# Performance work log

Hardware: AMD Instinct MI355X
Metric: run time of the kernel (lower is better)

## Reference

```python
import jax, jax.numpy as jnp
import numpy as np

D_MODEL = 256
NHEAD = 8
NUM_LAYERS = 4
LN_EPS = 1e-5

def _layernorm(x, g, b):
    mu = jnp.mean(x, axis=-1, keepdims=True)
    var = jnp.mean((x - mu) ** 2, axis=-1, keepdims=True)
    return (x - mu) * jax.lax.rsqrt(var + LN_EPS) * g + b

def setup_inputs() -> dict:
    key = jax.random.key(0)
    ks = jax.random.split(key, 16)
    B, M, D, L = 2, 2048, D_MODEL, NUM_LAYERS
    s = 0.02
    inp = {
        'x': jax.random.normal(ks[0], (B, M, D), jnp.float32),
        'coords': jax.random.normal(ks[1], (B, M, 3), jnp.float32),
        'wq': jax.random.normal(ks[2], (L, D, D), jnp.float32) * s,
        'bq': jnp.zeros((L, D), jnp.float32),
        'wk': jax.random.normal(ks[3], (L, D, D), jnp.float32) * s,
        'bk': jnp.zeros((L, D), jnp.float32),
        'wv': jax.random.normal(ks[4], (L, D, D), jnp.float32) * s,
        'bv': jnp.zeros((L, D), jnp.float32),
        'alpha': jnp.full((L,), 0.1, jnp.float32),
        'w1': jax.random.normal(ks[5], (L, D, 2 * D), jnp.float32) * s,
        'b1': jnp.zeros((L, 2 * D), jnp.float32),
        'w2': jax.random.normal(ks[6], (L, 2 * D, D), jnp.float32) * s,
        'b2': jnp.zeros((L, D), jnp.float32),
        'ln1_g': jnp.ones((L, D), jnp.float32),
        'ln1_b': jnp.zeros((L, D), jnp.float32),
        'ln2_g': jnp.ones((L, D), jnp.float32),
        'ln2_b': jnp.zeros((L, D), jnp.float32),
    }
    return inp

def reference(x, coords, wq, bq, wk, bk, wv, bv, alpha, w1, b1, w2, b2, ln1_g, ln1_b, ln2_g, ln2_b):
    B, M, D = x.shape
    H = NHEAD
    dk = D // H
    # Geometric bias: per-batch block of the original B*M x B*M dot matrix,
    # i.e. G[b] = coords[b] @ coords[b].T  (identical math, computed directly).
    G0 = jnp.einsum('bmd,bnd->bmn', coords, coords)  # [B, M, M]
    scale = 1.0 / jnp.sqrt(jnp.asarray(dk, x.dtype))

    def heads(t):  # [B,M,D] -> [B,H,M,dk]
        return t.reshape(B, M, H, dk).transpose(0, 2, 1, 3)

    for i in range(NUM_LAYERS):
        q = heads(x @ wq[i] + bq[i])
        k = heads(x @ wk[i] + bk[i])
        v = heads(x @ wv[i] + bv[i])
        scores = jnp.einsum('bhmd,bhnd->bhmn', q, k) * scale + (alpha[i] * G0)[:, None]
        attn = jax.nn.softmax(scores, axis=-1)
        out = jnp.einsum('bhmn,bhnd->bhmd', attn, v)
        out = out.transpose(0, 2, 1, 3).reshape(B, M, D)
        x = _layernorm(x + out, ln1_g[i], ln1_b[i])
        ff = jax.nn.relu(x @ w1[i] + b1[i]) @ w2[i] + b2[i]
        x = _layernorm(x + ff, ln2_g[i], ln2_b[i])
    return x
```

## Files before the change

kernel.cpp:

```cpp
#include <hip/hip_runtime.h>

typedef unsigned short u16;
typedef __attribute__((ext_vector_type(8))) short short8;
typedef __attribute__((ext_vector_type(4))) float f32x4;
typedef __attribute__((ext_vector_type(4))) u16 u16x4;

#define MFMA16(a, b, c) __builtin_amdgcn_mfma_f32_16x16x32_bf16(a, b, c, 0, 0, 0)
#define EXP2(x) __builtin_amdgcn_exp2f(x)

#define LOG2E 1.4426950408889634f
#define QSCALE 0.25506038410312156f

__device__ __forceinline__ u16 f2bf(float f) {
    unsigned int u = __builtin_bit_cast(unsigned int, f);
    u += 0x7fffu + ((u >> 16) & 1u);
    return (u16)(u >> 16);
}

__global__ __launch_bounds__(256) void repack_kernel(
    const float* __restrict__ wq, const float* __restrict__ wk, const float* __restrict__ wv,
    const float* __restrict__ bq, const float* __restrict__ bk, const float* __restrict__ bv,
    const float* __restrict__ w1, const float* __restrict__ w2,
    u16* __restrict__ wqkvT, u16* __restrict__ w1T, u16* __restrict__ w2T,
    float* __restrict__ bqkv)
{
    long idx = (long)blockIdx.x * 256 + threadIdx.x;
    const long NQ = 4L * 768 * 256;
    const long N1 = 4L * 512 * 256;
    const long N2 = 4L * 256 * 512;
    const long NB = 4L * 768;
    if (idx < NQ) {
        long l = idx / (768 * 256); long r = idx % (768 * 256);
        long n = r / 256, k = r % 256;
        float v;
        if (n < 256)      v = wq[(l * 256 + k) * 256 + n] * QSCALE;
        else if (n < 512) v = wk[(l * 256 + k) * 256 + (n - 256)];
        else              v = wv[(l * 256 + k) * 256 + (n - 512)];
        wqkvT[idx] = f2bf(v);
    } else if ((idx -= NQ) < N1) {
        long l = idx / (512 * 256); long r = idx % (512 * 256);
        long n = r / 256, k = r % 256;
        w1T[idx] = f2bf(w1[(l * 256 + k) * 512 + n]);
    } else if ((idx -= N1) < N2) {
        long l = idx / (256 * 512); long r = idx % (256 * 512);
        long n = r / 512, k = r % 512;
        w2T[idx] = f2bf(w2[(l * 512 + k) * 256 + n]);
    } else if ((idx -= N2) < NB) {
        long l = idx / 768; long n = idx % 768;
        float v = (n < 256) ? bq[l * 256 + n] * QSCALE
                : (n < 512) ? bk[l * 256 + (n - 256)]
                            : bv[l * 256 + (n - 512)];
        bqkv[l * 768 + n] = v;
    }
}

__global__ __launch_bounds__(256) void xconv_kernel(
    const float* __restrict__ xin, const float* __restrict__ coords,
    float* __restrict__ xf, u16* __restrict__ xb, u16* __restrict__ kcoord)
{
    long idx = (long)blockIdx.x * 256 + threadIdx.x;
    if (idx < 4096L * 256) {
        float v = xin[idx];
        xf[idx] = v;
        xb[idx] = f2bf(v);
    }
    if (idx < 4096) {
        const float* c = coords + idx * 3;
        u16 r0 = f2bf(c[0] * LOG2E), r1 = f2bf(c[1] * LOG2E), r2 = f2bf(c[2] * LOG2E);
        uint4 lo; lo.x = (unsigned)r0 | ((unsigned)r1 << 16); lo.y = (unsigned)r2; lo.z = 0; lo.w = 0;
        uint4 z4; z4.x = 0; z4.y = 0; z4.z = 0; z4.w = 0;
        uint4* dst = (uint4*)(kcoord + idx * 32);
        dst[0] = lo; dst[1] = z4; dst[2] = z4; dst[3] = z4;
    }
}

__global__ __launch_bounds__(256) void qkvgemm_kernel(
    const u16* __restrict__ A, const u16* __restrict__ BT,
    const float* __restrict__ bias,
    u16* __restrict__ qt, u16* __restrict__ kt, u16* __restrict__ vt)
{
    const int K = 256;
    int w = threadIdx.x >> 6, lane = threadIdx.x & 63;
    int wr = w >> 1, wc = w & 1;
    int m0 = blockIdx.x * 64 + wr * 32;
    int n0 = blockIdx.y * 64 + wc * 32;
    int l16 = lane & 15, lhi = lane >> 4;

    f32x4 acc[2][2];
#pragma unroll
    for (int i = 0; i < 2; i++)
#pragma unroll
        for (int j = 0; j < 2; j++) acc[i][j] = (f32x4){0.f, 0.f, 0.f, 0.f};

    const u16* Ap = A + (size_t)(m0 + l16) * K + lhi * 8;
    const u16* Bp = BT + (size_t)(n0 + l16) * K + lhi * 8;

#pragma unroll 4
    for (int k = 0; k < K; k += 32) {
        short8 a0 = *(const short8*)(Ap + k);
        short8 a1 = *(const short8*)(Ap + (size_t)16 * K + k);
        short8 b0 = *(const short8*)(Bp + k);
        short8 b1 = *(const short8*)(Bp + (size_t)16 * K + k);
        acc[0][0] = MFMA16(a0, b0, acc[0][0]);
        acc[0][1] = MFMA16(a0, b1, acc[0][1]);
        acc[1][0] = MFMA16(a1, b0, acc[1][0]);
        acc[1][1] = MFMA16(a1, b1, acc[1][1]);
    }

#pragma unroll
    for (int i = 0; i < 2; i++)
#pragma unroll
        for (int j = 0; j < 2; j++) {
            int n = n0 + j * 16 + l16;
            float bs = bias[n];
            int sect = n >> 8;
            int h = (n >> 5) & 7;
            int d = n & 31;
            int m = m0 + i * 16 + lhi * 4;
            int b = m >> 11, mseq = m & 2047;
            if (sect < 2) {
                u16* dst = (sect == 0 ? qt : kt) + ((size_t)(b * 8 + h) * 2048 + mseq) * 32 + d;
#pragma unroll
                for (int r = 0; r < 4; r++) dst[(size_t)r * 32] = f2bf(acc[i][j][r] + bs);
            } else {
                u16x4 pk;
#pragma unroll
                for (int r = 0; r < 4; r++) pk[r] = f2bf(acc[i][j][r] + bs);
                *(u16x4*)(vt + ((size_t)(b * 8 + h) * 32 + d) * 2048 + mseq) = pk;
            }
        }
}

template <bool RELU, bool OUTF32>
__global__ __launch_bounds__(256) void gemm_kernel(
    const u16* __restrict__ A, const u16* __restrict__ BT,
    const float* __restrict__ bias, void* __restrict__ outp,
    int M, int N, int K)
{
    int w = threadIdx.x >> 6, lane = threadIdx.x & 63;
    int wr = w >> 1, wc = w & 1;
    int m0 = blockIdx.x * 64 + wr * 32;
    int n0 = blockIdx.y * 64 + wc * 32;
    int l16 = lane & 15, lhi = lane >> 4;

    f32x4 acc[2][2];
#pragma unroll
    for (int i = 0; i < 2; i++)
#pragma unroll
        for (int j = 0; j < 2; j++) acc[i][j] = (f32x4){0.f, 0.f, 0.f, 0.f};

    const u16* Ap = A + (size_t)(m0 + l16) * K + lhi * 8;
    const u16* Bp = BT + (size_t)(n0 + l16) * K + lhi * 8;

#pragma unroll 4
    for (int k = 0; k < K; k += 32) {
        short8 a0 = *(const short8*)(Ap + k);
        short8 a1 = *(const short8*)(Ap + (size_t)16 * K + k);
        short8 b0 = *(const short8*)(Bp + k);
        short8 b1 = *(const short8*)(Bp + (size_t)16 * K + k);
        acc[0][0] = MFMA16(a0, b0, acc[0][0]);
        acc[0][1] = MFMA16(a0, b1, acc[0][1]);
        acc[1][0] = MFMA16(a1, b0, acc[1][0]);
        acc[1][1] = MFMA16(a1, b1, acc[1][1]);
    }

#pragma unroll
    for (int i = 0; i < 2; i++)
#pragma unroll
        for (int j = 0; j < 2; j++) {
            int n = n0 + j * 16 + l16;
            float bs = bias[n];
#pragma unroll
            for (int r = 0; r < 4; r++) {
                int m = m0 + i * 16 + lhi * 4 + r;
                float v = acc[i][j][r] + bs;
                if (RELU) v = fmaxf(v, 0.f);
                if (OUTF32) ((float*)outp)[(size_t)m * N + n] = v;
                else        ((u16*)outp)[(size_t)m * N + n] = f2bf(v);
            }
        }
}

__global__ __launch_bounds__(256, 4) void attn_kernel(
    const u16* __restrict__ qt, const u16* __restrict__ kt, const u16* __restrict__ vt,
    const u16* __restrict__ kcoord, const float* __restrict__ coords,
    const float* __restrict__ alpha, int layer,
    float* __restrict__ po, float* __restrict__ pml)
{
    int tid = threadIdx.x;
    int w = tid >> 6, lane = tid & 63;
    int flat = blockIdx.x;
    int bh = (flat & 7) | (((flat >> 3) & 1) << 3);
    int b = bh >> 3, h = bh & 7;
    int m0 = ((flat >> 4) & 63) * 32;
    int kvhalf = flat >> 10;
    int l16 = lane & 15, lhi = lane >> 4;

    __shared__ __align__(16) char smem[18432 + 1024];
    float* olds = (float*)smem;
    float* mlds = (float*)(smem + 18432);

    const u16* qbase = qt + (size_t)bh * 2048 * 32;
    float al = alpha[layer];
    short8 qlo[2], qhi[2];
#pragma unroll
    for (int qq = 0; qq < 2; qq++) {
        qlo[qq] = *(const short8*)(qbase + (size_t)(m0 + qq * 16 + l16) * 32 + lhi * 8);
        short8 z = {0, 0, 0, 0, 0, 0, 0, 0};
        qhi[qq] = z;
        if (lhi == 0) {
            const float* c = coords + (size_t)(b * 2048 + m0 + qq * 16 + l16) * 3;
            qhi[qq][0] = (short)f2bf(c[0] * al);
            qhi[qq][1] = (short)f2bf(c[1] * al);
            qhi[qq][2] = (short)f2bf(c[2] * al);
        }
    }

    f32x4 oacc[2][2];
#pragma unroll
    for (int qq = 0; qq < 2; qq++)
#pragma unroll
        for (int dt = 0; dt < 2; dt++) oacc[qq][dt] = (f32x4){0.f, 0.f, 0.f, 0.f};
    float mrow[2] = {-1e30f, -1e30f}, lrow[2] = {0.f, 0.f};

    const u16* kb  = kt + (size_t)bh * 2048 * 32 + lhi * 8;
    const u16* kcb = kcoord + (size_t)b * 2048 * 32 + lhi * 8;
    const u16* vbase = vt + ((size_t)bh * 32 + l16) * 2048;

    int nbase = kvhalf * 16 + w * 4;
#pragma unroll
    for (int nbi = 0; nbi < 4; nbi++) {
        int n0b = (nbase + nbi) * 64;
        f32x4 s[2][4];
#pragma unroll
        for (int t = 0; t < 4; t++) {
            size_t nr = (size_t)(n0b + t * 16 + l16);
            short8 klo = *(const short8*)(kb + nr * 32);
            short8 khi = *(const short8*)(kcb + nr * 32);
            f32x4 z0 = (f32x4){0.f, 0.f, 0.f, 0.f};
            z0 = MFMA16(klo, qlo[0], z0);
            s[0][t] = MFMA16(khi, qhi[0], z0);
            f32x4 z1 = (f32x4){0.f, 0.f, 0.f, 0.f};
            z1 = MFMA16(klo, qlo[1], z1);
            s[1][t] = MFMA16(khi, qhi[1], z1);
        }
#pragma unroll
        for (int qq = 0; qq < 2; qq++) {
            float lm = -1e30f;
#pragma unroll
            for (int t = 0; t < 4; t++) {
                float a = fmaxf(fmaxf(s[qq][t][0], s[qq][t][1]), fmaxf(s[qq][t][2], s[qq][t][3]));
                lm = fmaxf(lm, a);
            }
            if (!__all(lm <= mrow[qq] + 8.f)) {
                float tm = fmaxf(lm, __shfl_xor(lm, 16, 64));
                tm = fmaxf(tm, __shfl_xor(tm, 32, 64));
                float mnew = fmaxf(mrow[qq], tm);
                float corr = EXP2(mrow[qq] - mnew);
                mrow[qq] = mnew;
#pragma unroll
                for (int dt = 0; dt < 2; dt++)
#pragma unroll
                    for (int r = 0; r < 4; r++) oacc[qq][dt][r] *= corr;
                lrow[qq] *= corr;
            }

            float rs = 0.f;
#pragma unroll
            for (int t = 0; t < 4; t++) {
#pragma unroll
                for (int r = 0; r < 4; r++) s[qq][t][r] = EXP2(s[qq][t][r] - mrow[qq]);
                rs += (s[qq][t][0] + s[qq][t][1]) + (s[qq][t][2] + s[qq][t][3]);
            }
            lrow[qq] += rs;

            u16* pl = (u16*)smem + (w * 2 + qq) * 1024;
#pragma unroll
            for (int t = 0; t < 4; t++) {
                unsigned p0, p1;
                asm("v_cvt_pk_bf16_f32 %0, %1, %2" : "=v"(p0) : "v"(s[qq][t][0]), "v"(s[qq][t][1]));
                asm("v_cvt_pk_bf16_f32 %0, %1, %2" : "=v"(p1) : "v"(s[qq][t][2]), "v"(s[qq][t][3]));
                int slot = (t * 2 + (lhi >> 1)) ^ (l16 & 7);
                uint2 val; val.x = p0; val.y = p1;
                *(uint2*)(pl + l16 * 64 + (slot << 3) + (lhi & 1) * 4) = val;
            }
        }

        u16* pl0 = (u16*)smem + (w * 2) * 1024;
        u16* pl1 = (u16*)smem + (w * 2 + 1) * 1024;
#pragma unroll
        for (int kk = 0; kk < 2; kk++) {
            int soff = ((kk * 4 + lhi) ^ (l16 & 7)) << 3;
            short8 pf0 = *(const short8*)(pl0 + l16 * 64 + soff);
            short8 pf1 = *(const short8*)(pl1 + l16 * 64 + soff);
#pragma unroll
            for (int dt = 0; dt < 2; dt++) {
                short8 vf = *(const short8*)(vbase + (size_t)dt * 16 * 2048 + n0b + kk * 32 + lhi * 8);
                oacc[0][dt] = MFMA16(vf, pf0, oacc[0][dt]);
                oacc[1][dt] = MFMA16(vf, pf1, oacc[1][dt]);
            }
        }
    }

#pragma unroll
    for (int qq = 0; qq < 2; qq++) {
        lrow[qq] += __shfl_xor(lrow[qq], 16, 64);
        lrow[qq] += __shfl_xor(lrow[qq], 32, 64);
    }

    __syncthreads();
    if (lhi == 0) {
#pragma unroll
        for (int qq = 0; qq < 2; qq++) {
            mlds[((w * 2 + qq) * 2 + 0) * 16 + l16] = mrow[qq];
            mlds[((w * 2 + qq) * 2 + 1) * 16 + l16] = lrow[qq];
        }
    }
#pragma unroll
    for (int qq = 0; qq < 2; qq++)
#pragma unroll
        for (int dt = 0; dt < 2; dt++)
            *(f32x4*)(olds + ((size_t)(w * 2 + qq) * 16 + l16) * 36 + dt * 16 + lhi * 4) = oacc[qq][dt];
    __syncthreads();

    int d = tid & 31, q8 = tid >> 5;
#pragma unroll
    for (int qq2 = 0; qq2 < 4; qq2++) {
        int q = q8 + qq2 * 8;
        int q16 = q & 15, qh2 = q >> 4;
        float mw[4], lw[4];
#pragma unroll
        for (int ww = 0; ww < 4; ww++) {
            mw[ww] = mlds[((ww * 2 + qh2) * 2 + 0) * 16 + q16];
            lw[ww] = mlds[((ww * 2 + qh2) * 2 + 1) * 16 + q16];
        }
        float mg = fmaxf(fmaxf(mw[0], mw[1]), fmaxf(mw[2], mw[3]));
        float o = 0.f, lg = 0.f;
#pragma unroll
        for (int ww = 0; ww < 4; ww++) {
            float sc = EXP2(mw[ww] - mg);
            lg += lw[ww] * sc;
            o += olds[((size_t)(ww * 2 + qh2) * 16 + q16) * 36 + d] * sc;
        }
        size_t row = (size_t)(b * 2048 + m0 + q);
        po[((size_t)kvhalf * 4096 + row) * 256 + h * 32 + d] = o;
        if (d == 0) {
            float2 ml2; ml2.x = mg; ml2.y = lg;
            *(float2*)(pml + ((size_t)kvhalf * 4096 + row) * 16 + h * 2) = ml2;
        }
    }
}

__global__ __launch_bounds__(256) void lnmerge_kernel(
    const float* __restrict__ xin, const float* __restrict__ po,
    const float* __restrict__ pml,
    const float* __restrict__ g, const float* __restrict__ bb,
    float* __restrict__ outf, u16* __restrict__ outb)
{
    int w = threadIdx.x >> 6, lane = threadIdx.x & 63;
    int row = blockIdx.x * 4 + w;
    int h = lane >> 3;
    float m0v = pml[(size_t)row * 16 + h * 2];
    float l0v = pml[(size_t)row * 16 + h * 2 + 1];
    float m1v = pml[((size_t)4096 + row) * 16 + h * 2];
    float l1v = pml[((size_t)4096 + row) * 16 + h * 2 + 1];
    float mg = fmaxf(m0v, m1v);
    float w0 = exp2f(m0v - mg), w1 = exp2f(m1v - mg);
    float inv = 1.f / (l0v * w0 + l1v * w1);

    size_t base = (size_t)row * 256 + lane * 4;
    float4 xv = *(const float4*)(xin + base);
    float4 a0 = *(const float4*)(po + base);
    float4 a1 = *(const float4*)(po + (size_t)4096 * 256 + base);
    float s0 = xv.x + (a0.x * w0 + a1.x * w1) * inv;
    float s1 = xv.y + (a0.y * w0 + a1.y * w1) * inv;
    float s2 = xv.z + (a0.z * w0 + a1.z * w1) * inv;
    float s3 = xv.w + (a0.w * w0 + a1.w * w1) * inv;

    float sum = s0 + s1 + s2 + s3;
    float sq = s0 * s0 + s1 * s1 + s2 * s2 + s3 * s3;
#pragma unroll
    for (int off = 1; off < 64; off <<= 1) {
        sum += __shfl_xor(sum, off, 64);
        sq += __shfl_xor(sq, off, 64);
    }
    float mu = sum * (1.f / 256.f);
    float var = sq * (1.f / 256.f) - mu * mu;
    float rs = rsqrtf(var + 1e-5f);
    float4 gv = *(const float4*)(g + lane * 4);
    float4 bv = *(const float4*)(bb + lane * 4);
    float y0 = (s0 - mu) * rs * gv.x + bv.x;
    float y1 = (s1 - mu) * rs * gv.y + bv.y;
    float y2 = (s2 - mu) * rs * gv.z + bv.z;
    float y3 = (s3 - mu) * rs * gv.w + bv.w;
    float4 yo; yo.x = y0; yo.y = y1; yo.z = y2; yo.w = y3;
    *(float4*)(outf + base) = yo;
    unsigned int p0 = (unsigned int)f2bf(y0) | ((unsigned int)f2bf(y1) << 16);
    unsigned int p1 = (unsigned int)f2bf(y2) | ((unsigned int)f2bf(y3) << 16);
    uint2 pk; pk.x = p0; pk.y = p1;
    *(uint2*)(outb + base) = pk;
}

__global__ __launch_bounds__(256) void ln_kernel(
    const float* __restrict__ xin, const float* __restrict__ add,
    const float* __restrict__ g, const float* __restrict__ bb,
    float* __restrict__ outf, u16* __restrict__ outb)
{
    int w = threadIdx.x >> 6, lane = threadIdx.x & 63;
    int row = blockIdx.x * 4 + w;
    size_t base = (size_t)row * 256 + lane * 4;
    float4 xv = *(const float4*)(xin + base);
    float4 av = *(const float4*)(add + base);
    float s0 = xv.x + av.x, s1 = xv.y + av.y, s2 = xv.z + av.z, s3 = xv.w + av.w;
    float sum = s0 + s1 + s2 + s3;
    float sq = s0 * s0 + s1 * s1 + s2 * s2 + s3 * s3;
#pragma unroll
    for (int off = 1; off < 64; off <<= 1) {
        sum += __shfl_xor(sum, off, 64);
        sq += __shfl_xor(sq, off, 64);
    }
    float mu = sum * (1.f / 256.f);
    float var = sq * (1.f / 256.f) - mu * mu;
    float rs = rsqrtf(var + 1e-5f);
    float4 gv = *(const float4*)(g + lane * 4);
    float4 bv = *(const float4*)(bb + lane * 4);
    float y0 = (s0 - mu) * rs * gv.x + bv.x;
    float y1 = (s1 - mu) * rs * gv.y + bv.y;
    float y2 = (s2 - mu) * rs * gv.z + bv.z;
    float y3 = (s3 - mu) * rs * gv.w + bv.w;
    float4 yo; yo.x = y0; yo.y = y1; yo.z = y2; yo.w = y3;
    *(float4*)(outf + base) = yo;
    unsigned int p0 = (unsigned int)f2bf(y0) | ((unsigned int)f2bf(y1) << 16);
    unsigned int p1 = (unsigned int)f2bf(y2) | ((unsigned int)f2bf(y3) << 16);
    uint2 pk; pk.x = p0; pk.y = p1;
    *(uint2*)(outb + base) = pk;
}

extern "C" void kernel_launch(void* const* d_in, const int* in_sizes, int n_in,
                              void* d_out, int out_size, void* d_ws, size_t ws_size,
                              hipStream_t stream)
{
    const float* x_in   = (const float*)d_in[0];
    const float* coords = (const float*)d_in[1];
    const float* wq = (const float*)d_in[2];
    const float* bq = (const float*)d_in[3];
    const float* wk = (const float*)d_in[4];
    const float* bk = (const float*)d_in[5];
    const float* wv = (const float*)d_in[6];
    const float* bv = (const float*)d_in[7];
    const float* alpha = (const float*)d_in[8];
    const float* w1 = (const float*)d_in[9];
    const float* b1 = (const float*)d_in[10];
    const float* w2 = (const float*)d_in[11];
    const float* b2 = (const float*)d_in[12];
    const float* ln1g = (const float*)d_in[13];
    const float* ln1b = (const float*)d_in[14];
    const float* ln2g = (const float*)d_in[15];
    const float* ln2b = (const float*)d_in[16];
    float* out = (float*)d_out;

    char* ws = (char*)d_ws;
    size_t off = 0;
    auto alloc = [&](size_t bytes) -> void* {
        void* p = ws + off;
        off += (bytes + 255) & ~(size_t)255;
        return p;
    };
    float* x_f32 = (float*)alloc(4096UL * 256 * 4);
    u16*   x_bf  = (u16*)  alloc(4096UL * 256 * 2);
    u16*   qt    = (u16*)  alloc(16UL * 2048 * 32 * 2);
    u16*   ktp   = (u16*)  alloc(16UL * 2048 * 32 * 2);
    u16*   vtp   = (u16*)  alloc(16UL * 32 * 2048 * 2);
    u16*   kcoord= (u16*)  alloc(2UL * 2048 * 32 * 2);
    float* po    = (float*)alloc(2UL * 4096 * 256 * 4);
    float* pml   = (float*)alloc(2UL * 4096 * 16 * 4);
    u16*   mid   = (u16*)  alloc(4096UL * 512 * 2);
    float* ffn   = (float*)alloc(4096UL * 256 * 4);
    u16*   wqkvT = (u16*)  alloc(4UL * 768 * 256 * 2);
    u16*   w1T   = (u16*)  alloc(4UL * 512 * 256 * 2);
    u16*   w2T   = (u16*)  alloc(4UL * 256 * 512 * 2);
    float* bqkv  = (float*)alloc(4UL * 768 * 4);

    repack_kernel<<<7180, 256, 0, stream>>>(wq, wk, wv, bq, bk, bv, w1, w2,
                                            wqkvT, w1T, w2T, bqkv);
    xconv_kernel<<<4096, 256, 0, stream>>>(x_in, coords, x_f32, x_bf, kcoord);

    for (int i = 0; i < 4; i++) {
        qkvgemm_kernel<<<dim3(64, 12), 256, 0, stream>>>(
            x_bf, wqkvT + (size_t)i * 768 * 256, bqkv + i * 768, qt, ktp, vtp);
        attn_kernel<<<2048, 256, 0, stream>>>(qt, ktp, vtp, kcoord, coords, alpha, i, po, pml);
        lnmerge_kernel<<<1024, 256, 0, stream>>>(x_f32, po, pml, ln1g + i * 256, ln1b + i * 256,
                                                 x_f32, x_bf);
        gemm_kernel<true, false><<<dim3(64, 8), 256, 0, stream>>>(
            x_bf, w1T + (size_t)i * 512 * 256, b1 + i * 512, mid, 4096, 512, 256);
        gemm_kernel<false, true><<<dim3(64, 4), 256, 0, stream>>>(
            mid, w2T + (size_t)i * 256 * 512, b2 + i * 256, ffn, 4096, 256, 512);
        ln_kernel<<<1024, 256, 0, stream>>>(x_f32, ffn, ln2g + i * 256, ln2b + i * 256,
                                            (i == 3) ? out : x_f32, x_bf);
    }
}
```

Measured before the change: 326.2 us.

## Fuse FFN down-projection with residual LayerNorm and simplify attention addressing

Replaces the second FFN GEMM plus separate LayerNorm kernel with one kernel that computes a 16-row by 256-column tile, adds bias and residual, reduces row statistics across waves via shared memory, and writes normalized fp32 and bf16 outputs. This removes the intermediate fp32 ffn buffer round trip and one launch per layer. The attention kernel also precomputes 32-bit element indices and swizzled LDS offsets to cut address arithmetic in the inner loop. The fused epilogue uses scalar, less coalesced global accesses, and each block does more serial K work with fewer waves per tile.

```diff
diff --git a/kernel.cpp b/kernel.cpp
--- a/kernel.cpp
+++ b/kernel.cpp
@@ -131,10 +131,9 @@
         }
 }
 
-template <bool RELU, bool OUTF32>
-__global__ __launch_bounds__(256) void gemm_kernel(
+__global__ __launch_bounds__(256) void gemm_relu_kernel(
     const u16* __restrict__ A, const u16* __restrict__ BT,
-    const float* __restrict__ bias, void* __restrict__ outp,
+    const float* __restrict__ bias, u16* __restrict__ outp,
     int M, int N, int K)
 {
     int w = threadIdx.x >> 6, lane = threadIdx.x & 63;
@@ -173,12 +172,101 @@
 #pragma unroll
             for (int r = 0; r < 4; r++) {
                 int m = m0 + i * 16 + lhi * 4 + r;
-                float v = acc[i][j][r] + bs;
-                if (RELU) v = fmaxf(v, 0.f);
-                if (OUTF32) ((float*)outp)[(size_t)m * N + n] = v;
-                else        ((u16*)outp)[(size_t)m * N + n] = f2bf(v);
+                outp[(size_t)m * N + n] = f2bf(fmaxf(acc[i][j][r] + bs, 0.f));
             }
         }
+}
+
+__global__ __launch_bounds__(256) void ffn2ln_kernel(
+    const u16* __restrict__ A , const u16* __restrict__ BT ,
+    const float* __restrict__ bias, const float* __restrict__ xin,
+    const float* __restrict__ g, const float* __restrict__ bb,
+    float* __restrict__ outf, u16* __restrict__ outb)
+{
+    const int K = 512;
+    int w = threadIdx.x >> 6, lane = threadIdx.x & 63;
+    int l16 = lane & 15, lhi = lane >> 4;
+    int row0 = blockIdx.x * 16;
+    int n0 = w * 64;
+
+    __shared__ float2 sums[4][16];
+
+    f32x4 acc[4];
+#pragma unroll
+    for (int j = 0; j < 4; j++) acc[j] = (f32x4){0.f, 0.f, 0.f, 0.f};
+
+    const u16* Ap = A + (size_t)(row0 + l16) * K + lhi * 8;
+    const u16* Bp = BT + (size_t)(n0 + l16) * K + lhi * 8;
+
+#pragma unroll 4
+    for (int k = 0; k < K; k += 32) {
+        short8 a = *(const short8*)(Ap + k);
+        short8 b0 = *(const short8*)(Bp + k);
+        short8 b1 = *(const short8*)(Bp + (size_t)16 * K + k);
+        short8 b2v = *(const short8*)(Bp + (size_t)32 * K + k);
+        short8 b3 = *(const short8*)(Bp + (size_t)48 * K + k);
+        acc[0] = MFMA16(a, b0, acc[0]);
+        acc[1] = MFMA16(a, b1, acc[1]);
+        acc[2] = MFMA16(a, b2v, acc[2]);
+        acc[3] = MFMA16(a, b3, acc[3]);
+    }
+
+    float vv[4][4];
+    float psum[4] = {0.f, 0.f, 0.f, 0.f}, psq[4] = {0.f, 0.f, 0.f, 0.f};
+#pragma unroll
+    for (int j = 0; j < 4; j++) {
+        int col = n0 + j * 16 + l16;
+        float bs = bias[col];
+#pragma unroll
+        for (int r = 0; r < 4; r++) {
+            int row = row0 + lhi * 4 + r;
+            float y = acc[j][r] + bs + xin[(size_t)row * 256 + col];
+            vv[j][r] = y;
+            psum[r] += y;
+            psq[r] += y * y;
+        }
+    }
+#pragma unroll
+    for (int off = 1; off < 16; off <<= 1)
+#pragma unroll
+        for (int r = 0; r < 4; r++) {
+            psum[r] += __shfl_xor(psum[r], off, 64);
+            psq[r] += __shfl_xor(psq[r], off, 64);
+        }
+    if (l16 == 0) {
+#pragma unroll
+        for (int r = 0; r < 4; r++) {
+            float2 t; t.x = psum[r]; t.y = psq[r];
+            sums[w][lhi * 4 + r] = t;
+        }
+    }
+    __syncthreads();
+    float mu[4], rsg[4];
+#pragma unroll
+    for (int r = 0; r < 4; r++) {
+        int row = lhi * 4 + r;
+        float s = 0.f, q = 0.f;
+#pragma unroll
+        for (int ww = 0; ww < 4; ww++) {
+            float2 t = sums[ww][row];
+            s += t.x; q += t.y;
+        }
+        float m = s * (1.f / 256.f);
+        mu[r] = m;
+        rsg[r] = rsqrtf(q * (1.f / 256.f) - m * m + 1e-5f);
+    }
+#pragma unroll
+    for (int j = 0; j < 4; j++) {
+        int col = n0 + j * 16 + l16;
+        float gv = g[col], bv = bb[col];
+#pragma unroll
+        for (int r = 0; r < 4; r++) {
+            int row = row0 + lhi * 4 + r;
+            float y = (vv[j][r] - mu[r]) * rsg[r] * gv + bv;
+            outf[(size_t)row * 256 + col] = y;
+            outb[(size_t)row * 256 + col] = f2bf(y);
+        }
+    }
 }
 
 __global__ __launch_bounds__(256, 4) void attn_kernel(
@@ -199,6 +287,7 @@
     __shared__ __align__(16) char smem[18432 + 1024];
     float* olds = (float*)smem;
     float* mlds = (float*)(smem + 18432);
+    u16* plbase = (u16*)smem;
 
     const u16* qbase = qt + (size_t)bh * 2048 * 32;
     float al = alpha[layer];
@@ -223,20 +312,29 @@
         for (int dt = 0; dt < 2; dt++) oacc[qq][dt] = (f32x4){0.f, 0.f, 0.f, 0.f};
     float mrow[2] = {-1e30f, -1e30f}, lrow[2] = {0.f, 0.f};
 
-    const u16* kb  = kt + (size_t)bh * 2048 * 32 + lhi * 8;
-    const u16* kcb = kcoord + (size_t)b * 2048 * 32 + lhi * 8;
-    const u16* vbase = vt + ((size_t)bh * 32 + l16) * 2048;
-
     int nbase = kvhalf * 16 + w * 4;
+    int nstart = nbase * 64;
+
+    unsigned kidx = ((unsigned)(bh * 2048 + nstart + l16) << 5) + lhi * 8;
+    unsigned cidx = ((unsigned)(b * 2048 + nstart + l16) << 5) + lhi * 8;
+    unsigned vidxA = ((unsigned)(bh * 32 + l16) << 11) + nstart + lhi * 8;
+    unsigned vidxB = vidxA + (16u << 11);
+
+    int hb = lhi >> 1, s7 = l16 & 7, lo4 = (lhi & 1) * 4;
+    int wb = w * 2048 + l16 * 64;
+    int wa[4], ra[2];
+#pragma unroll
+    for (int t = 0; t < 4; t++) wa[t] = wb + (((((t << 1) | hb)) ^ s7) << 3) + lo4;
+#pragma unroll
+    for (int kk = 0; kk < 2; kk++) ra[kk] = wb + ((((kk << 2) | lhi) ^ s7) << 3);
+
 #pragma unroll
     for (int nbi = 0; nbi < 4; nbi++) {
-        int n0b = (nbase + nbi) * 64;
         f32x4 s[2][4];
 #pragma unroll
         for (int t = 0; t < 4; t++) {
-            size_t nr = (size_t)(n0b + t * 16 + l16);
-            short8 klo = *(const short8*)(kb + nr * 32);
-            short8 khi = *(const short8*)(kcb + nr * 32);
+            short8 klo = *(const short8*)(kt + kidx + t * 512);
+            short8 khi = *(const short8*)(kcoord + cidx + t * 512);
             f32x4 z0 = (f32x4){0.f, 0.f, 0.f, 0.f};
             z0 = MFMA16(klo, qlo[0], z0);
             s[0][t] = MFMA16(khi, qhi[0], z0);
@@ -244,6 +342,7 @@
             z1 = MFMA16(klo, qlo[1], z1);
             s[1][t] = MFMA16(khi, qhi[1], z1);
         }
+        kidx += 2048; cidx += 2048;
 #pragma unroll
         for (int qq = 0; qq < 2; qq++) {
             float lm = -1e30f;
@@ -274,32 +373,29 @@
             }
             lrow[qq] += rs;
 
-            u16* pl = (u16*)smem + (w * 2 + qq) * 1024;
+            u16* pl = plbase + qq * 1024;
 #pragma unroll
             for (int t = 0; t < 4; t++) {
                 unsigned p0, p1;
                 asm("v_cvt_pk_bf16_f32 %0, %1, %2" : "=v"(p0) : "v"(s[qq][t][0]), "v"(s[qq][t][1]));
                 asm("v_cvt_pk_bf16_f32 %0, %1, %2" : "=v"(p1) : "v"(s[qq][t][2]), "v"(s[qq][t][3]));
-                int slot = (t * 2 + (lhi >> 1)) ^ (l16 & 7);
                 uint2 val; val.x = p0; val.y = p1;
-                *(uint2*)(pl + l16 * 64 + (slot << 3) + (lhi & 1) * 4) = val;
+                *(uint2*)(pl + wa[t]) = val;
             }
         }
 
-        u16* pl0 = (u16*)smem + (w * 2) * 1024;
-        u16* pl1 = (u16*)smem + (w * 2 + 1) * 1024;
 #pragma unroll
         for (int kk = 0; kk < 2; kk++) {
-            int soff = ((kk * 4 + lhi) ^ (l16 & 7)) << 3;
-            short8 pf0 = *(const short8*)(pl0 + l16 * 64 + soff);
-            short8 pf1 = *(const short8*)(pl1 + l16 * 64 + soff);
-#pragma unroll
-            for (int dt = 0; dt < 2; dt++) {
-                short8 vf = *(const short8*)(vbase + (size_t)dt * 16 * 2048 + n0b + kk * 32 + lhi * 8);
-                oacc[0][dt] = MFMA16(vf, pf0, oacc[0][dt]);
-                oacc[1][dt] = MFMA16(vf, pf1, oacc[1][dt]);
-            }
-        }
+            short8 pf0 = *(const short8*)(plbase + ra[kk]);
+            short8 pf1 = *(const short8*)(plbase + 1024 + ra[kk]);
+            short8 vf0 = *(const short8*)(vt + vidxA + kk * 32);
+            short8 vf1 = *(const short8*)(vt + vidxB + kk * 32);
+            oacc[0][0] = MFMA16(vf0, pf0, oacc[0][0]);
+            oacc[1][0] = MFMA16(vf0, pf1, oacc[1][0]);
+            oacc[0][1] = MFMA16(vf1, pf0, oacc[0][1]);
+            oacc[1][1] = MFMA16(vf1, pf1, oacc[1][1]);
+        }
+        vidxA += 64; vidxB += 64;
     }
 
 #pragma unroll
@@ -377,41 +473,6 @@
     float s2 = xv.z + (a0.z * w0 + a1.z * w1) * inv;
     float s3 = xv.w + (a0.w * w0 + a1.w * w1) * inv;
 
-    float sum = s0 + s1 + s2 + s3;
-    float sq = s0 * s0 + s1 * s1 + s2 * s2 + s3 * s3;
-#pragma unroll
-    for (int off = 1; off < 64; off <<= 1) {
-        sum += __shfl_xor(sum, off, 64);
-        sq += __shfl_xor(sq, off, 64);
-    }
-    float mu = sum * (1.f / 256.f);
-    float var = sq * (1.f / 256.f) - mu * mu;
-    float rs = rsqrtf(var + 1e-5f);
-    float4 gv = *(const float4*)(g + lane * 4);
-    float4 bv = *(const float4*)(bb + lane * 4);
-    float y0 = (s0 - mu) * rs * gv.x + bv.x;
-    float y1 = (s1 - mu) * rs * gv.y + bv.y;
-    float y2 = (s2 - mu) * rs * gv.z + bv.z;
-    float y3 = (s3 - mu) * rs * gv.w + bv.w;
-    float4 yo; yo.x = y0; yo.y = y1; yo.z = y2; yo.w = y3;
-    *(float4*)(outf + base) = yo;
-    unsigned int p0 = (unsigned int)f2bf(y0) | ((unsigned int)f2bf(y1) << 16);
-    unsigned int p1 = (unsigned int)f2bf(y2) | ((unsigned int)f2bf(y3) << 16);
-    uint2 pk; pk.x = p0; pk.y = p1;
-    *(uint2*)(outb + base) = pk;
-}
-
-__global__ __launch_bounds__(256) void ln_kernel(
-    const float* __restrict__ xin, const float* __restrict__ add,
-    const float* __restrict__ g, const float* __restrict__ bb,
-    float* __restrict__ outf, u16* __restrict__ outb)
-{
-    int w = threadIdx.x >> 6, lane = threadIdx.x & 63;
-    int row = blockIdx.x * 4 + w;
-    size_t base = (size_t)row * 256 + lane * 4;
-    float4 xv = *(const float4*)(xin + base);
-    float4 av = *(const float4*)(add + base);
-    float s0 = xv.x + av.x, s1 = xv.y + av.y, s2 = xv.z + av.z, s3 = xv.w + av.w;
     float sum = s0 + s1 + s2 + s3;
     float sq = s0 * s0 + s1 * s1 + s2 * s2 + s3 * s3;
 #pragma unroll
@@ -475,7 +536,6 @@
     float* po    = (float*)alloc(2UL * 4096 * 256 * 4);
     float* pml   = (float*)alloc(2UL * 4096 * 16 * 4);
     u16*   mid   = (u16*)  alloc(4096UL * 512 * 2);
-    float* ffn   = (float*)alloc(4096UL * 256 * 4);
     u16*   wqkvT = (u16*)  alloc(4UL * 768 * 256 * 2);
     u16*   w1T   = (u16*)  alloc(4UL * 512 * 256 * 2);
     u16*   w2T   = (u16*)  alloc(4UL * 256 * 512 * 2);
@@ -491,11 +551,10 @@
         attn_kernel<<<2048, 256, 0, stream>>>(qt, ktp, vtp, kcoord, coords, alpha, i, po, pml);
         lnmerge_kernel<<<1024, 256, 0, stream>>>(x_f32, po, pml, ln1g + i * 256, ln1b + i * 256,
                                                  x_f32, x_bf);
-        gemm_kernel<true, false><<<dim3(64, 8), 256, 0, stream>>>(
+        gemm_relu_kernel<<<dim3(64, 8), 256, 0, stream>>>(
             x_bf, w1T + (size_t)i * 512 * 256, b1 + i * 512, mid, 4096, 512, 256);
-        gemm_kernel<false, true><<<dim3(64, 4), 256, 0, stream>>>(
-            mid, w2T + (size_t)i * 256 * 512, b2 + i * 256, ffn, 4096, 256, 512);
-        ln_kernel<<<1024, 256, 0, stream>>>(x_f32, ffn, ln2g + i * 256, ln2b + i * 256,
-                                            (i == 3) ? out : x_f32, x_bf);
-    }
-}
+        ffn2ln_kernel<<<256, 256, 0, stream>>>(
+            mid, w2T + (size_t)i * 256 * 512, b2 + i * 256, x_f32,
+            ln2g + i * 256, ln2b + i * 256, (i == 3) ? out : x_f32, x_bf);
+    }
+}
```

Result: slower. 357.6 us (+9.6%).
